# Kernel optimization log

Hardware: AMD Instinct MI355X
Metric: run time of the kernel (lower is better)

Reference implementation:

```python
import jax, jax.numpy as jnp
import numpy as np

DEPTH = 16                      # complete binary tree depth (root level = DEPTH)
NUM_LEVELS = DEPTH + 1          # node_order in [0, DEPTH]
N_NODES = 2 ** (DEPTH + 1) - 1  # 131071
VOCAB = 50000
EMB = 128
HID = 128


def setup_inputs() -> dict:
    key = jax.random.key(0)
    ks = jax.random.split(key, 6)
    # --- deterministic complete binary tree structure ---
    idx = np.arange(N_NODES)
    depth = np.floor(np.log2(idx + 1)).astype(np.int64)  # root idx 0 has depth 0
    node_order = (DEPTH - depth).astype(np.int64)        # leaves evaluated first (order 0)
    internal = np.arange(2 ** DEPTH - 1)                 # nodes with children
    parents = np.repeat(internal, 2)                     # consecutive grouping per parent
    children = np.stack([2 * internal + 1, 2 * internal + 2], axis=1).ravel()
    adjacency_list = np.stack([parents, children], axis=1).astype(np.int64)
    edge_order = node_order[parents]
    s = 0.02
    return {
        "features": jax.random.randint(ks[0], (N_NODES,), 0, VOCAB),
        "node_order": jnp.asarray(node_order),
        "adjacency_list": jnp.asarray(adjacency_list),
        "edge_order": jnp.asarray(edge_order),
        "emb": jax.random.normal(ks[1], (VOCAB, EMB), jnp.float32) * s,
        "W_iou": jax.random.normal(ks[2], (EMB, 3 * HID), jnp.float32) * s,
        "b_iou": jnp.zeros((3 * HID,), jnp.float32),
        "U_iou": jax.random.normal(ks[3], (HID, 3 * HID), jnp.float32) * s,
        "W_f": jax.random.normal(ks[4], (EMB, HID), jnp.float32) * s,
        "b_f": jnp.zeros((HID,), jnp.float32),
        "U_f": jax.random.normal(ks[5], (HID, HID), jnp.float32) * s,
    }


def reference(features, node_order, adjacency_list, edge_order,
              emb, W_iou, b_iou, U_iou, W_f, b_f, U_f):
    x = emb[features]                                   # [N, EMB] embedding lookup
    par = adjacency_list[:, 0]                          # [E]
    chd = adjacency_list[:, 1]                          # [E]
    Wx = x @ W_iou + b_iou                              # [N, 3H] input contributions (precomputed)
    Wfx = x @ W_f + b_f                                 # [N, H] forget-gate input term
    N = x.shape[0]
    H = W_f.shape[1]
    h = jnp.zeros((N, H), x.dtype)
    c = jnp.zeros((N, H), x.dtype)
    # level-synchronous TreeLSTM: leaves (level 0) up to root
    for lvl in range(NUM_LEVELS):
        nmask = (node_order == lvl)[:, None]            # nodes updated this level
        emask = (edge_order == lvl)[:, None].astype(x.dtype)  # edges feeding them
        child_h = h[chd]                                # [E, H] gather children
        child_c = c[chd]
        h_sum = jax.ops.segment_sum(child_h * emask, par, num_segments=N)  # [N, H]
        iou = Wx + h_sum @ U_iou                        # [N, 3H]
        i, o, u = jnp.split(iou, 3, axis=1)
        i = jax.nn.sigmoid(i)
        o = jax.nn.sigmoid(o)
        u = jnp.tanh(u)
        f = jax.nn.sigmoid(Wfx[par] + child_h @ U_f)    # [E, H] per-edge forget gate
        c_sum = jax.ops.segment_sum(f * child_c * emask, par, num_segments=N)
        c_new = i * u + c_sum                           # level 0: c_sum == 0 -> i*u (leaf branch)
        c = jnp.where(nmask, c_new, c)
        h = jnp.where(nmask, o * jnp.tanh(c_new), h)
    return h, c
```

## Files before the change

kernel.cpp:

```cpp
#include <hip/hip_runtime.h>
#include <math.h>

#define NN 131071
#define HD 128
#define N_INTERNAL 65535
#define LEAF_BASE 65535

typedef short bf16x8 __attribute__((ext_vector_type(8)));
typedef unsigned short u16x8 __attribute__((ext_vector_type(8)));
typedef unsigned short u16x4 __attribute__((ext_vector_type(4)));
typedef float f32x4 __attribute__((ext_vector_type(4)));

__device__ __forceinline__ float sigm(float z) { return 1.0f / (1.0f + __expf(-z)); }
__device__ __forceinline__ float tanh_f(float z) { return 1.0f - 2.0f / (__expf(2.0f * z) + 1.0f); }

__device__ __forceinline__ unsigned short f2bf(float f) {
    unsigned u = __float_as_uint(f);
    u += 0x7FFFu + ((u >> 16) & 1u);
    return (unsigned short)(u >> 16);
}
__device__ __forceinline__ float bf2f(unsigned short b) {
    return __uint_as_float(((unsigned)b) << 16);
}

__device__ __forceinline__ f32x4 mfma16(bf16x8 a, bf16x8 b, f32x4 c) {
    return __builtin_amdgcn_mfma_f32_16x16x32_bf16(a, b, c, 0, 0, 0);
}

__device__ __forceinline__ float4 addf4(float4 a, float4 b) {
    float4 r; r.x = a.x + b.x; r.y = a.y + b.y; r.z = a.z + b.z; r.w = a.w + b.w; return r;
}

__device__ __forceinline__ void lds_store8(unsigned short* region, int r, int cc, float4 a, float4 b) {
    u16x8 p;
    p[0] = f2bf(a.x); p[1] = f2bf(a.y); p[2] = f2bf(a.z); p[3] = f2bf(a.w);
    p[4] = f2bf(b.x); p[5] = f2bf(b.y); p[6] = f2bf(b.z); p[7] = f2bf(b.w);
    *(u16x8*)&region[r * HD + ((cc ^ (r & 7)) << 3)] = p;
}

__device__ __forceinline__ bf16x8 lds_frag(const unsigned short* region, int row, int ks, int kl) {
    int cc = ks * 4 + kl;
    return *(const bf16x8*)&region[row * HD + ((cc ^ (row & 7)) << 3)];
}

__device__ __forceinline__ bf16x8 frag2(const unsigned short* M, int ct, int ks, int lane) {
    return *(const bf16x8*)&M[(((ct * 4 + ks) * 64) + lane) * 8];
}

__global__ __launch_bounds__(256) void build_packed(
    const float* __restrict__ W_iou, const float* __restrict__ U_iou,
    const float* __restrict__ W_f, const float* __restrict__ U_f,
    unsigned short* __restrict__ ws)
{
    int f = blockIdx.x * 256 + threadIdx.x;
    int mat = f >> 13;
    int rem = f & 8191;
    int ct = rem >> 8;
    int ks = (rem >> 6) & 3;
    int lane = rem & 63;
    int col = ct * 16 + (lane & 15);
    int k0 = ks * 32 + (lane >> 4) * 8;
    u16x8 out;
#pragma unroll
    for (int e = 0; e < 8; ++e) {
        int k = k0 + e;
        float v;
        if (mat == 0) v = (col < 384) ? W_iou[k * 384 + col] : W_f[k * HD + (col - 384)];
        else          v = (col < 384) ? U_iou[k * 384 + col] : U_f[k * HD + (col - 384)];
        out[e] = f2bf(v);
    }
    *(u16x8*)&ws[(size_t)f * 8] = out;
}

__global__ __launch_bounds__(512) void xp_leaf_kernel(
    const int* __restrict__ feat, const float* __restrict__ emb,
    const unsigned short* __restrict__ WT2,
    const float* __restrict__ b_iou, const float* __restrict__ b_f,
    unsigned short* __restrict__ XPb, float* __restrict__ hbuf, float* __restrict__ cbuf)
{
    __shared__ unsigned short ldsx[64 * HD];
    const int t = threadIdx.x;
    const int m0 = blockIdx.x * 64;
    {
        int r = t >> 3, c8 = t & 7;
        int n = m0 + r;
        int nn = n < NN ? n : 0;
        const float* sx = emb + (size_t)feat[nn] * HD + c8 * 16;
        float4 x0 = *(const float4*)(sx + 0);
        float4 x1 = *(const float4*)(sx + 4);
        float4 x2 = *(const float4*)(sx + 8);
        float4 x3 = *(const float4*)(sx + 12);
        lds_store8(ldsx, r, c8 * 2 + 0, x0, x1);
        lds_store8(ldsx, r, c8 * 2 + 1, x2, x3);
    }
    __syncthreads();

    const int lane = t & 63, w = t >> 6;
    const int jq = w & 3, mh = w >> 2;
    const int l15 = lane & 15, kl = lane >> 4;

    f32x4 zero = {0.f, 0.f, 0.f, 0.f};
    f32x4 acc[4][2][2];
#pragma unroll
    for (int g = 0; g < 4; ++g)
#pragma unroll
        for (int mp = 0; mp < 2; ++mp)
#pragma unroll
            for (int jt = 0; jt < 2; ++jt) acc[g][mp][jt] = zero;

#pragma unroll
    for (int ks = 0; ks < 4; ++ks) {
        bf16x8 a0 = lds_frag(ldsx, (mh * 2 + 0) * 16 + l15, ks, kl);
        bf16x8 a1 = lds_frag(ldsx, (mh * 2 + 1) * 16 + l15, ks, kl);
#pragma unroll
        for (int g = 0; g < 4; ++g) {
#pragma unroll
            for (int jt = 0; jt < 2; ++jt) {
                bf16x8 b = frag2(WT2, g * 8 + jq * 2 + jt, ks, lane);
                acc[g][0][jt] = mfma16(a0, b, acc[g][0][jt]);
                acc[g][1][jt] = mfma16(a1, b, acc[g][1][jt]);
            }
        }
    }

#pragma unroll
    for (int mp = 0; mp < 2; ++mp) {
#pragma unroll
        for (int jt = 0; jt < 2; ++jt) {
            int j = jq * 32 + jt * 16 + l15;
            int nb = m0 + (mh * 2 + mp) * 16 + kl * 4;
            float bi = b_iou[j], bo = b_iou[HD + j], bu = b_iou[2 * HD + j], bf = b_f[j];
#pragma unroll
            for (int r = 0; r < 4; ++r) {
                int n = nb + r;
                if (n >= NN) continue;
                if (n >= LEAF_BASE) {
                    float iv = sigm(acc[0][mp][jt][r] + bi);
                    float ov = sigm(acc[1][mp][jt][r] + bo);
                    float uv = tanh_f(acc[2][mp][jt][r] + bu);
                    float cv = iv * uv;
                    cbuf[(size_t)n * HD + j] = cv;
                    hbuf[(size_t)n * HD + j] = ov * tanh_f(cv);
                } else {
                    u16x4 pk;
                    pk[0] = f2bf(acc[0][mp][jt][r] + bi);
                    pk[1] = f2bf(acc[1][mp][jt][r] + bo);
                    pk[2] = f2bf(acc[2][mp][jt][r] + bu);
                    pk[3] = f2bf(acc[3][mp][jt][r] + bf);
                    *(u16x4*)&XPb[((size_t)n * HD + j) * 4] = pk;
                }
            }
        }
    }
}

__device__ __forceinline__ void level_body(
    unsigned short* lds,
    const unsigned short* __restrict__ UT2, const unsigned short* __restrict__ XPb,
    float* __restrict__ hbuf, float* __restrict__ cbuf, int base, int count, int m0)
{
    unsigned short* ldshs = lds;
    unsigned short* ldsh1 = lds + 8192;
    unsigned short* ldsh2 = lds + 16384;

    const int t = threadIdx.x;
    {
        int r = t >> 3, c8 = t & 7;
        int row = m0 + r;
        int n = base + (row < count ? row : 0);
        const float* s1 = hbuf + (size_t)(2 * n + 1) * HD + c8 * 16;
        const float* s2 = hbuf + (size_t)(2 * n + 2) * HD + c8 * 16;
        float4 p0 = *(const float4*)(s1 + 0);
        float4 p1 = *(const float4*)(s1 + 4);
        float4 p2 = *(const float4*)(s1 + 8);
        float4 p3 = *(const float4*)(s1 + 12);
        float4 q0 = *(const float4*)(s2 + 0);
        float4 q1 = *(const float4*)(s2 + 4);
        float4 q2 = *(const float4*)(s2 + 8);
        float4 q3 = *(const float4*)(s2 + 12);
        lds_store8(ldsh1, r, c8 * 2 + 0, p0, p1);
        lds_store8(ldsh1, r, c8 * 2 + 1, p2, p3);
        lds_store8(ldsh2, r, c8 * 2 + 0, q0, q1);
        lds_store8(ldsh2, r, c8 * 2 + 1, q2, q3);
        lds_store8(ldshs, r, c8 * 2 + 0, addf4(p0, q0), addf4(p1, q1));
        lds_store8(ldshs, r, c8 * 2 + 1, addf4(p2, q2), addf4(p3, q3));
    }
    __syncthreads();

    const int lane = t & 63, w = t >> 6;
    const int jq = w & 3, mh = w >> 2;
    const int l15 = lane & 15, kl = lane >> 4;

    f32x4 zero = {0.f, 0.f, 0.f, 0.f};
    f32x4 acc[5][2][2];
#pragma unroll
    for (int g = 0; g < 5; ++g)
#pragma unroll
        for (int mp = 0; mp < 2; ++mp)
#pragma unroll
            for (int jt = 0; jt < 2; ++jt) acc[g][mp][jt] = zero;

#pragma unroll
    for (int ks = 0; ks < 4; ++ks) {
        bf16x8 ahs0 = lds_frag(ldshs, (mh * 2 + 0) * 16 + l15, ks, kl);
        bf16x8 ahs1 = lds_frag(ldshs, (mh * 2 + 1) * 16 + l15, ks, kl);
        bf16x8 ah10 = lds_frag(ldsh1, (mh * 2 + 0) * 16 + l15, ks, kl);
        bf16x8 ah11 = lds_frag(ldsh1, (mh * 2 + 1) * 16 + l15, ks, kl);
        bf16x8 ah20 = lds_frag(ldsh2, (mh * 2 + 0) * 16 + l15, ks, kl);
        bf16x8 ah21 = lds_frag(ldsh2, (mh * 2 + 1) * 16 + l15, ks, kl);
#pragma unroll
        for (int jt = 0; jt < 2; ++jt) {
            bf16x8 Bi = frag2(UT2,  0 + jq * 2 + jt, ks, lane);
            bf16x8 Bo = frag2(UT2,  8 + jq * 2 + jt, ks, lane);
            bf16x8 Bu = frag2(UT2, 16 + jq * 2 + jt, ks, lane);
            bf16x8 Bf = frag2(UT2, 24 + jq * 2 + jt, ks, lane);
            acc[0][0][jt] = mfma16(ahs0, Bi, acc[0][0][jt]);
            acc[0][1][jt] = mfma16(ahs1, Bi, acc[0][1][jt]);
            acc[1][0][jt] = mfma16(ahs0, Bo, acc[1][0][jt]);
            acc[1][1][jt] = mfma16(ahs1, Bo, acc[1][1][jt]);
            acc[2][0][jt] = mfma16(ahs0, Bu, acc[2][0][jt]);
            acc[2][1][jt] = mfma16(ahs1, Bu, acc[2][1][jt]);
            acc[3][0][jt] = mfma16(ah10, Bf, acc[3][0][jt]);
            acc[3][1][jt] = mfma16(ah11, Bf, acc[3][1][jt]);
            acc[4][0][jt] = mfma16(ah20, Bf, acc[4][0][jt]);
            acc[4][1][jt] = mfma16(ah21, Bf, acc[4][1][jt]);
        }
    }

#pragma unroll
    for (int mp = 0; mp < 2; ++mp) {
#pragma unroll
        for (int jt = 0; jt < 2; ++jt) {
            int j = jq * 32 + jt * 16 + l15;
#pragma unroll
            for (int r = 0; r < 4; ++r) {
                int row = m0 + (mh * 2 + mp) * 16 + kl * 4 + r;
                if (row >= count) continue;
                int n = base + row;
                u16x4 pk = *(const u16x4*)&XPb[((size_t)n * HD + j) * 4];
                float iv = sigm(acc[0][mp][jt][r] + bf2f(pk[0]));
                float ov = sigm(acc[1][mp][jt][r] + bf2f(pk[1]));
                float uv = tanh_f(acc[2][mp][jt][r] + bf2f(pk[2]));
                float fx = bf2f(pk[3]);
                float f1 = sigm(acc[3][mp][jt][r] + fx);
                float f2 = sigm(acc[4][mp][jt][r] + fx);
                float c1 = cbuf[(size_t)(2 * n + 1) * HD + j];
                float c2 = cbuf[(size_t)(2 * n + 2) * HD + j];
                float cn = fmaf(iv, uv, fmaf(f1, c1, f2 * c2));
                cbuf[(size_t)n * HD + j] = cn;
                hbuf[(size_t)n * HD + j] = ov * tanh_f(cn);
            }
        }
    }
}

__global__ __launch_bounds__(512) void level_u_kernel(
    const unsigned short* __restrict__ UT2, const unsigned short* __restrict__ XPb,
    float* __restrict__ hbuf, float* __restrict__ cbuf, int base, int count)
{
    __shared__ unsigned short lds[3 * 64 * HD];
    level_body(lds, UT2, XPb, hbuf, cbuf, base, count, blockIdx.x * 64);
}

__global__ __launch_bounds__(512) void tail_kernel(
    const unsigned short* __restrict__ UT2, const unsigned short* __restrict__ XPb,
    float* __restrict__ hbuf, float* __restrict__ cbuf)
{
    __shared__ unsigned short lds[3 * 64 * HD];
    for (int lvl = 9; lvl <= 16; ++lvl) {
        const int count = 1 << (16 - lvl);
        const int base = count - 1;
        for (int m0 = 0; m0 < count; m0 += 64) {
            level_body(lds, UT2, XPb, hbuf, cbuf, base, count, m0);
            __syncthreads();
        }
    }
}

template <int MT>
__global__ __launch_bounds__(128) void leaf_kernel(
    const int* __restrict__ feat, const float* __restrict__ emb,
    const float* __restrict__ W_iou, const float* __restrict__ b_iou,
    float* __restrict__ hbuf, float* __restrict__ cbuf, int base)
{
    __shared__ float X[MT][HD];
    const int j = threadIdx.x;
    const int m0 = blockIdx.x * MT;
#pragma unroll
    for (int m = 0; m < MT; ++m) {
        int n = base + m0 + m;
        X[m][j] = emb[(size_t)feat[n] * HD + j];
    }
    __syncthreads();
    float ai[MT], ao[MT], au[MT];
#pragma unroll
    for (int m = 0; m < MT; ++m) {
        ai[m] = b_iou[j]; ao[m] = b_iou[HD + j]; au[m] = b_iou[2 * HD + j];
    }
#pragma unroll 4
    for (int k = 0; k < HD; ++k) {
        float wi = W_iou[k * 3 * HD + j];
        float wo = W_iou[k * 3 * HD + HD + j];
        float wu = W_iou[k * 3 * HD + 2 * HD + j];
#pragma unroll
        for (int m = 0; m < MT; ++m) {
            float x = X[m][k];
            ai[m] = fmaf(x, wi, ai[m]); ao[m] = fmaf(x, wo, ao[m]); au[m] = fmaf(x, wu, au[m]);
        }
    }
#pragma unroll
    for (int m = 0; m < MT; ++m) {
        int n = base + m0 + m;
        float iv = sigm(ai[m]); float ov = sigm(ao[m]); float uv = tanh_f(au[m]);
        float cv = iv * uv;
        cbuf[(size_t)n * HD + j] = cv;
        hbuf[(size_t)n * HD + j] = ov * tanh_f(cv);
    }
}

template <int MT>
__global__ __launch_bounds__(128) void level_kernel(
    const int* __restrict__ feat, const float* __restrict__ emb,
    const float* __restrict__ W_iou, const float* __restrict__ b_iou,
    const float* __restrict__ U_iou,
    const float* __restrict__ W_f, const float* __restrict__ b_f,
    const float* __restrict__ U_f,
    float* __restrict__ hbuf, float* __restrict__ cbuf, int base)
{
    __shared__ float X[MT][HD];
    __shared__ float H1[MT][HD];
    __shared__ float H2[MT][HD];
    const int j = threadIdx.x;
    const int m0 = blockIdx.x * MT;
#pragma unroll
    for (int m = 0; m < MT; ++m) {
        int n = base + m0 + m;
        X[m][j]  = emb[(size_t)feat[n] * HD + j];
        H1[m][j] = hbuf[(size_t)(2 * n + 1) * HD + j];
        H2[m][j] = hbuf[(size_t)(2 * n + 2) * HD + j];
    }
    __syncthreads();
    float ai[MT], ao[MT], au[MT], g1[MT], g2[MT];
#pragma unroll
    for (int m = 0; m < MT; ++m) {
        ai[m] = b_iou[j]; ao[m] = b_iou[HD + j]; au[m] = b_iou[2 * HD + j];
        g1[m] = b_f[j]; g2[m] = b_f[j];
    }
#pragma unroll 2
    for (int k = 0; k < HD; ++k) {
        float wi = W_iou[k * 3 * HD + j];
        float wo = W_iou[k * 3 * HD + HD + j];
        float wu = W_iou[k * 3 * HD + 2 * HD + j];
        float ui = U_iou[k * 3 * HD + j];
        float uo = U_iou[k * 3 * HD + HD + j];
        float uu = U_iou[k * 3 * HD + 2 * HD + j];
        float wf = W_f[k * HD + j];
        float uf = U_f[k * HD + j];
#pragma unroll
        for (int m = 0; m < MT; ++m) {
            float x = X[m][k]; float h1 = H1[m][k]; float h2 = H2[m][k]; float hs = h1 + h2;
            ai[m] = fmaf(x, wi, fmaf(hs, ui, ai[m]));
            ao[m] = fmaf(x, wo, fmaf(hs, uo, ao[m]));
            au[m] = fmaf(x, wu, fmaf(hs, uu, au[m]));
            g1[m] = fmaf(x, wf, fmaf(h1, uf, g1[m]));
            g2[m] = fmaf(x, wf, fmaf(h2, uf, g2[m]));
        }
    }
#pragma unroll
    for (int m = 0; m < MT; ++m) {
        int n = base + m0 + m;
        float iv = sigm(ai[m]); float ov = sigm(ao[m]); float uv = tanh_f(au[m]);
        float f1 = sigm(g1[m]); float f2 = sigm(g2[m]);
        float c1 = cbuf[(size_t)(2 * n + 1) * HD + j];
        float c2 = cbuf[(size_t)(2 * n + 2) * HD + j];
        float cn = fmaf(iv, uv, fmaf(f1, c1, f2 * c2));
        cbuf[(size_t)n * HD + j] = cn;
        hbuf[(size_t)n * HD + j] = ov * tanh_f(cn);
    }
}

extern "C" void kernel_launch(void* const* d_in, const int* in_sizes, int n_in,
                              void* d_out, int out_size, void* d_ws, size_t ws_size,
                              hipStream_t stream)
{
    const int*   feat  = (const int*)d_in[0];
    const float* emb   = (const float*)d_in[4];
    const float* W_iou = (const float*)d_in[5];
    const float* b_iou = (const float*)d_in[6];
    const float* U_iou = (const float*)d_in[7];
    const float* W_f   = (const float*)d_in[8];
    const float* b_f   = (const float*)d_in[9];
    const float* U_f   = (const float*)d_in[10];

    float* hbuf = (float*)d_out;
    float* cbuf = hbuf + (size_t)NN * HD;

    const size_t PACK_BYTES = 2u * 65536u * 2u;
    const size_t XP_BYTES   = (size_t)N_INTERNAL * HD * 4 * 2;
    if (ws_size >= PACK_BYTES + XP_BYTES) {
        unsigned short* wpk = (unsigned short*)d_ws;
        const unsigned short* WT2 = wpk;
        const unsigned short* UT2 = wpk + 65536;
        unsigned short* XPb = (unsigned short*)((char*)d_ws + PACK_BYTES);

        build_packed<<<64, 256, 0, stream>>>(W_iou, U_iou, W_f, U_f, wpk);
        xp_leaf_kernel<<<2048, 512, 0, stream>>>(feat, emb, WT2, b_iou, b_f, XPb, hbuf, cbuf);

        for (int lvl = 1; lvl <= 8; ++lvl) {
            const int count = 1 << (16 - lvl);
            const int base  = count - 1;
            level_u_kernel<<<count / 64, 512, 0, stream>>>(UT2, XPb, hbuf, cbuf, base, count);
        }
        tail_kernel<<<1, 512, 0, stream>>>(UT2, XPb, hbuf, cbuf);
    } else {
        leaf_kernel<16><<<65536 / 16, 128, 0, stream>>>(feat, emb, W_iou, b_iou, hbuf, cbuf, 65535);
        for (int lvl = 1; lvl <= 16; ++lvl) {
            const int d = 16 - lvl;
            const int count = 1 << d;
            const int base = count - 1;
            if (count >= 16) {
                level_kernel<16><<<count / 16, 128, 0, stream>>>(
                    feat, emb, W_iou, b_iou, U_iou, W_f, b_f, U_f, hbuf, cbuf, base);
            } else if (count == 8) {
                level_kernel<8><<<1, 128, 0, stream>>>(
                    feat, emb, W_iou, b_iou, U_iou, W_f, b_f, U_f, hbuf, cbuf, base);
            } else if (count == 4) {
                level_kernel<4><<<1, 128, 0, stream>>>(
                    feat, emb, W_iou, b_iou, U_iou, W_f, b_f, U_f, hbuf, cbuf, base);
            } else if (count == 2) {
                level_kernel<2><<<1, 128, 0, stream>>>(
                    feat, emb, W_iou, b_iou, U_iou, W_f, b_f, U_f, hbuf, cbuf, base);
            } else {
                level_kernel<1><<<1, 128, 0, stream>>>(
                    feat, emb, W_iou, b_iou, U_iou, W_f, b_f, U_f, hbuf, cbuf, base);
            }
        }
    }
}
```

Baseline: 309.6 us.

## Rewrite single-block tail kernel to feed MFMA from registers, not LDS

Replaces the single-block tail kernel, which reused the LDS-staged level_body, with a register-direct version. Child h rows are loaded from global memory, packed to bf16 fragments and fed straight to MFMA, with each wave handling 32 rows by 32 columns per gate. Level 9 moves out of the tail into a separate level_u_kernel launch. This is meant to cut LDS staging and barrier overhead on the serial top levels. The cost is one more launch and redundant clamped-row loads for small levels.

```diff
diff --git a/kernel.cpp b/kernel.cpp
--- a/kernel.cpp
+++ b/kernel.cpp
@@ -29,6 +29,13 @@
 
 __device__ __forceinline__ float4 addf4(float4 a, float4 b) {
     float4 r; r.x = a.x + b.x; r.y = a.y + b.y; r.z = a.z + b.z; r.w = a.w + b.w; return r;
+}
+
+__device__ __forceinline__ bf16x8 pk8(float4 a, float4 b) {
+    u16x8 p;
+    p[0] = f2bf(a.x); p[1] = f2bf(a.y); p[2] = f2bf(a.z); p[3] = f2bf(a.w);
+    p[4] = f2bf(b.x); p[5] = f2bf(b.y); p[6] = f2bf(b.z); p[7] = f2bf(b.w);
+    return *(bf16x8*)&p;
 }
 
 __device__ __forceinline__ void lds_store8(unsigned short* region, int r, int cc, float4 a, float4 b) {
@@ -262,18 +269,92 @@
     level_body(lds, UT2, XPb, hbuf, cbuf, base, count, blockIdx.x * 64);
 }
 
-__global__ __launch_bounds__(512) void tail_kernel(
+__global__ __launch_bounds__(512) void tail_kernel2(
     const unsigned short* __restrict__ UT2, const unsigned short* __restrict__ XPb,
     float* __restrict__ hbuf, float* __restrict__ cbuf)
 {
-    __shared__ unsigned short lds[3 * 64 * HD];
-    for (int lvl = 9; lvl <= 16; ++lvl) {
+    const int t = threadIdx.x;
+    const int lane = t & 63, w = t >> 6;
+    const int jq = w & 3, mh = w >> 2;
+    const int l15 = lane & 15, kl = lane >> 4;
+
+    for (int lvl = 10; lvl <= 16; ++lvl) {
         const int count = 1 << (16 - lvl);
         const int base = count - 1;
-        for (int m0 = 0; m0 < count; m0 += 64) {
-            level_body(lds, UT2, XPb, hbuf, cbuf, base, count, m0);
-            __syncthreads();
-        }
+        if (mh * 32 < count) {
+            f32x4 zero = {0.f, 0.f, 0.f, 0.f};
+            f32x4 acc[5][2][2];
+#pragma unroll
+            for (int g = 0; g < 5; ++g)
+#pragma unroll
+                for (int mp = 0; mp < 2; ++mp)
+#pragma unroll
+                    for (int jt = 0; jt < 2; ++jt) acc[g][mp][jt] = zero;
+
+#pragma unroll
+            for (int ks = 0; ks < 4; ++ks) {
+                bf16x8 ahs[2], ah1[2], ah2[2];
+#pragma unroll
+                for (int mp = 0; mp < 2; ++mp) {
+                    int row = mh * 32 + mp * 16 + l15;
+                    int rr = row < count ? row : count - 1;
+                    int n = base + rr;
+                    const float* p1 = hbuf + (size_t)(2 * n + 1) * HD + ks * 32 + kl * 8;
+                    const float* p2 = hbuf + (size_t)(2 * n + 2) * HD + ks * 32 + kl * 8;
+                    float4 a0 = *(const float4*)p1;
+                    float4 a1 = *(const float4*)(p1 + 4);
+                    float4 b0 = *(const float4*)p2;
+                    float4 b1 = *(const float4*)(p2 + 4);
+                    ah1[mp] = pk8(a0, a1);
+                    ah2[mp] = pk8(b0, b1);
+                    ahs[mp] = pk8(addf4(a0, b0), addf4(a1, b1));
+                }
+#pragma unroll
+                for (int jt = 0; jt < 2; ++jt) {
+                    bf16x8 Bi = frag2(UT2,  0 + jq * 2 + jt, ks, lane);
+                    bf16x8 Bo = frag2(UT2,  8 + jq * 2 + jt, ks, lane);
+                    bf16x8 Bu = frag2(UT2, 16 + jq * 2 + jt, ks, lane);
+                    bf16x8 Bf = frag2(UT2, 24 + jq * 2 + jt, ks, lane);
+                    acc[0][0][jt] = mfma16(ahs[0], Bi, acc[0][0][jt]);
+                    acc[0][1][jt] = mfma16(ahs[1], Bi, acc[0][1][jt]);
+                    acc[1][0][jt] = mfma16(ahs[0], Bo, acc[1][0][jt]);
+                    acc[1][1][jt] = mfma16(ahs[1], Bo, acc[1][1][jt]);
+                    acc[2][0][jt] = mfma16(ahs[0], Bu, acc[2][0][jt]);
+                    acc[2][1][jt] = mfma16(ahs[1], Bu, acc[2][1][jt]);
+                    acc[3][0][jt] = mfma16(ah1[0], Bf, acc[3][0][jt]);
+                    acc[3][1][jt] = mfma16(ah1[1], Bf, acc[3][1][jt]);
+                    acc[4][0][jt] = mfma16(ah2[0], Bf, acc[4][0][jt]);
+                    acc[4][1][jt] = mfma16(ah2[1], Bf, acc[4][1][jt]);
+                }
+            }
+
+#pragma unroll
+            for (int mp = 0; mp < 2; ++mp) {
+#pragma unroll
+                for (int jt = 0; jt < 2; ++jt) {
+                    int j = jq * 32 + jt * 16 + l15;
+#pragma unroll
+                    for (int r = 0; r < 4; ++r) {
+                        int row = mh * 32 + mp * 16 + kl * 4 + r;
+                        if (row >= count) continue;
+                        int n = base + row;
+                        u16x4 pk = *(const u16x4*)&XPb[((size_t)n * HD + j) * 4];
+                        float iv = sigm(acc[0][mp][jt][r] + bf2f(pk[0]));
+                        float ov = sigm(acc[1][mp][jt][r] + bf2f(pk[1]));
+                        float uv = tanh_f(acc[2][mp][jt][r] + bf2f(pk[2]));
+                        float fx = bf2f(pk[3]);
+                        float f1 = sigm(acc[3][mp][jt][r] + fx);
+                        float f2 = sigm(acc[4][mp][jt][r] + fx);
+                        float c1 = cbuf[(size_t)(2 * n + 1) * HD + j];
+                        float c2 = cbuf[(size_t)(2 * n + 2) * HD + j];
+                        float cn = fmaf(iv, uv, fmaf(f1, c1, f2 * c2));
+                        cbuf[(size_t)n * HD + j] = cn;
+                        hbuf[(size_t)n * HD + j] = ov * tanh_f(cn);
+                    }
+                }
+            }
+        }
+        __syncthreads();
     }
 }
 
@@ -406,12 +487,12 @@
         build_packed<<<64, 256, 0, stream>>>(W_iou, U_iou, W_f, U_f, wpk);
         xp_leaf_kernel<<<2048, 512, 0, stream>>>(feat, emb, WT2, b_iou, b_f, XPb, hbuf, cbuf);
 
-        for (int lvl = 1; lvl <= 8; ++lvl) {
+        for (int lvl = 1; lvl <= 9; ++lvl) {
             const int count = 1 << (16 - lvl);
             const int base  = count - 1;
             level_u_kernel<<<count / 64, 512, 0, stream>>>(UT2, XPb, hbuf, cbuf, base, count);
         }
-        tail_kernel<<<1, 512, 0, stream>>>(UT2, XPb, hbuf, cbuf);
+        tail_kernel2<<<1, 512, 0, stream>>>(UT2, XPb, hbuf, cbuf);
     } else {
         leaf_kernel<16><<<65536 / 16, 128, 0, stream>>>(feat, emb, W_iou, b_iou, hbuf, cbuf, 65535);
         for (int lvl = 1; lvl <= 16; ++lvl) {
```

Result: no change. 308.8 us (-0.3%).
